# Optimization experiments

Hardware: AMD Instinct MI355X
Metric: run time of the kernel (lower is better)

The kernel has to match this reference:

```python
import jax, jax.numpy as jnp
import numpy as np

B, N, C, H, DFF = 4, 1024, 768, 12, 3072
D = C // H
EPS = 1e-5


def _layernorm(x, w, b, axes):
    mu = jnp.mean(x, axis=axes, keepdims=True)
    var = jnp.mean(jnp.square(x - mu), axis=axes, keepdims=True)
    return (x - mu) * jax.lax.rsqrt(var + EPS) * w + b


def setup_inputs() -> dict:
    key = jax.random.key(0)
    ks = jax.random.split(key, 8)
    s = lambda fan_in: 1.0 / np.sqrt(fan_in)
    return {
        'x': jax.random.normal(ks[0], (B, N, C), jnp.float32),
        'ln0_w': jnp.ones((C,), jnp.float32),
        'ln0_b': jnp.zeros((C,), jnp.float32),
        'qkv_w': jax.random.normal(ks[1], (3 * C, C), jnp.float32) * s(C),
        'qkv_b': jax.random.normal(ks[2], (3 * C,), jnp.float32) * 0.01,
        'proj_w': jax.random.normal(ks[3], (C, C), jnp.float32) * s(C),
        'proj_b': jax.random.normal(ks[4], (C,), jnp.float32) * 0.01,
        'attn_norm_w': jnp.ones((H, N, N), jnp.float32),
        'attn_norm_b': jnp.zeros((H, N, N), jnp.float32),
        'ln1_w': jnp.ones((C,), jnp.float32),
        'ln1_b': jnp.zeros((C,), jnp.float32),
        'fc1_w': jax.random.normal(ks[5], (DFF, C), jnp.float32) * s(C),
        'fc1_b': jax.random.normal(ks[6], (DFF,), jnp.float32) * 0.01,
        'fc2_w': jax.random.normal(ks[7], (C, DFF), jnp.float32) * s(DFF),
        'fc2_b': jnp.zeros((C,), jnp.float32),
    }


def reference(x, ln0_w, ln0_b, qkv_w, qkv_b, proj_w, proj_b,
              attn_norm_w, attn_norm_b, ln1_w, ln1_b,
              fc1_w, fc1_b, fc2_w, fc2_b):
    # pre-norm
    h = _layernorm(x, ln0_w, ln0_b, axes=-1)
    # qkv projection -> (3, B, H, N, D)
    qkv = (h @ qkv_w.T + qkv_b).reshape(B, N, 3, H, D).transpose(2, 0, 3, 1, 4)
    q, k, v = qkv[0], qkv[1], qkv[2]
    # grassmanian_point: project each head vector onto the unit sphere
    q = q / jnp.linalg.norm(q, axis=-1, keepdims=True)
    k = k / jnp.linalg.norm(k, axis=-1, keepdims=True)
    # sum_d (q_{id} k_{jd})^2  ==  (q^2) @ (k^2)^T   -- avoids (B,H,D,N,N) tensor
    attn = jnp.einsum('bhid,bhjd->bhij', jnp.square(q), jnp.square(k))
    # LayerNorm over (H, N, N) jointly per batch element
    attn = _layernorm(attn, attn_norm_w, attn_norm_b, axes=(1, 2, 3))
    out = jnp.einsum('bhij,bhjd->bhid', attn, v)
    out = out.transpose(0, 2, 1, 3).reshape(B, N, C)
    out = out @ proj_w.T + proj_b
    # residual + post-norm + FFN (dropout/drop_path are identity in eval)
    src = x + out
    src = _layernorm(src, ln1_w, ln1_b, axes=-1)
    ff = jax.nn.gelu(src @ fc1_w.T + fc1_b, approximate=False) @ fc2_w.T + fc2_b
    src = src + ff
    return src, attn
```

## Files before the change

kernel.cpp:

```cpp
#include <hip/hip_runtime.h>

typedef __bf16 bf16;
typedef __bf16 bf16x4 __attribute__((ext_vector_type(4)));
typedef __bf16 bf16x8 __attribute__((ext_vector_type(8)));
typedef float f32x4 __attribute__((ext_vector_type(4)));

#define DEVI __device__ __forceinline__

typedef const __attribute__((address_space(1))) void* gas1;
typedef __attribute__((address_space(3))) void* las3;

DEVI int xcd_chunk(int bid, int nwg)
{
  const int q = nwg >> 3, r = nwg & 7;
  const int xcd = bid & 7, rank = bid >> 3;
  return (xcd < r) ? xcd * (q + 1) + rank
                   : r * (q + 1) + (xcd - r) * q + rank;
}

DEVI void stage_tile(const bf16* g, int ld, char* lds, int bytes, int tid)
{
  const int wv = tid >> 6, lane = tid & 63;
  const char* gb = (const char*)g;
  const long rowb = (long)ld * 2;
  for (int off = wv * 1024; off < bytes; off += 4096) {
    const int o  = off + lane * 16;
    const int s  = o ^ (((o >> 7) & 7) << 4);
    const int r  = s >> 7;
    const int cb = s & 127;
    __builtin_amdgcn_global_load_lds((gas1)(gb + (long)r * rowb + cb),
                                     (las3)(lds + off), 16, 0, 0);
  }
}

template<int N> DEVI void waitvm()
{
  if constexpr (N == 8)      asm volatile("s_waitcnt vmcnt(8)" ::: "memory");
  else if constexpr (N == 6) asm volatile("s_waitcnt vmcnt(6)" ::: "memory");
  else if constexpr (N == 4) asm volatile("s_waitcnt vmcnt(4)" ::: "memory");
  else if constexpr (N == 2) asm volatile("s_waitcnt vmcnt(2)" ::: "memory");
  else                       asm volatile("s_waitcnt vmcnt(0)" ::: "memory");
}

DEVI void wave_lds_fence()
{
  asm volatile("s_waitcnt lgkmcnt(0)" ::: "memory");
  __builtin_amdgcn_sched_barrier(0);
}

struct EpiProj {
  const float* bias; const float* x; float* src;
  DEVI void operator()(int z, int row, int col, float v) const {
    const long i = (long)row * 768 + col;
    src[i] = v + bias[col] + x[i];
  }
};

struct EpiGelu {
  const float* bias; bf16* g;
  DEVI void operator()(int z, int row, int col, float v) const {
    const float t = v + bias[col];
    const float r = 0.5f * t * (1.0f + erff(t * 0.70710678118654752f));
    g[(long)row * 3072 + col] = (bf16)r;
  }
};

struct EpiOut {
  const float* bias; const float* lnf; float* outp;
  DEVI void operator()(int z, int row, int col, float v) const {
    const long i = (long)row * 768 + col;
    outp[i] = v + bias[col] + lnf[i];
  }
};

template<int BM, int BN, int WC, int FM, int FN, int WPE, class Epi>
__global__ __launch_bounds__(256, WPE) void gemm_k(
    const bf16* __restrict__ A, long abatch,
    const bf16* __restrict__ B, long bbatch,
    int lda, int ldb, int K, Epi epi)
{
  constexpr int BK = 64;
  constexpr int AB = BM * BK * 2, BB = BN * BK * 2;
  constexpr int BUFB = AB + BB;
  constexpr int LPS = BUFB / 4096;
  __shared__ char smem[2 * BUFB];

  const int tid = threadIdx.x, lane = tid & 63, wv = tid >> 6;
  const int wr = wv / WC, wc = wv % WC;
  const int NT = gridDim.x;
  const int nwg = NT * gridDim.y;
  const int wid = xcd_chunk(blockIdx.y * NT + blockIdx.x, nwg);
  const int mt = wid / NT, nt = wid % NT;
  const int z = blockIdx.z;
  const long abase = (long)z * abatch + (long)mt * BM * lda;
  const long bbase = (long)z * bbatch + (long)nt * BN * ldb;
  const int l15 = lane & 15;
  const int sw = (lane & 7) << 4;

  auto stage_all = [&](int buf, int kt) {
    char* base = smem + buf * BUFB;
    stage_tile(A + abase + kt, lda, base, AB, tid);
    stage_tile(B + bbase + kt, ldb, base + AB, BB, tid);
  };

  f32x4 acc[FM][FN];
#pragma unroll
  for (int m = 0; m < FM; ++m)
#pragma unroll
    for (int n = 0; n < FN; ++n) acc[m][n] = f32x4{0.f, 0.f, 0.f, 0.f};

  const int arow = wr * FM * 16, bcol = wc * FN * 16;
  const int T = K / BK;

  stage_all(0, 0);
  int cur = 0;
  for (int t = 0; t < T; ++t) {
    if (t + 1 < T) { stage_all(cur ^ 1, (t + 1) * BK); waitvm<LPS>(); }
    else           { waitvm<0>(); }
    __builtin_amdgcn_s_barrier();
    asm volatile("" ::: "memory");

    const char* As = smem + cur * BUFB;
    const char* Bs = As + AB;
#pragma unroll
    for (int ks = 0; ks < 2; ++ks) {
      const int ko = (ks * 64 + (lane >> 4) * 16) ^ sw;
      bf16x8 av[FM], bv[FN];
#pragma unroll
      for (int m = 0; m < FM; ++m)
        av[m] = *(const bf16x8*)(As + (arow + m * 16 + l15) * 128 + ko);
#pragma unroll
      for (int n = 0; n < FN; ++n)
        bv[n] = *(const bf16x8*)(Bs + (bcol + n * 16 + l15) * 128 + ko);
#pragma unroll
      for (int m = 0; m < FM; ++m)
#pragma unroll
        for (int n = 0; n < FN; ++n)
          acc[m][n] = __builtin_amdgcn_mfma_f32_16x16x32_bf16(av[m], bv[n], acc[m][n], 0, 0, 0);
    }
    asm volatile("s_waitcnt lgkmcnt(0)" ::: "memory");
    __builtin_amdgcn_s_barrier();
    asm volatile("" ::: "memory");
    cur ^= 1;
  }

#pragma unroll
  for (int m = 0; m < FM; ++m)
#pragma unroll
    for (int n = 0; n < FN; ++n)
#pragma unroll
      for (int r = 0; r < 4; ++r) {
        const int grow = mt * BM + arow + m * 16 + (lane >> 4) * 4 + r;
        const int gcol = nt * BN + bcol + n * 16 + l15;
        epi(z, grow, gcol, acc[m][n][r]);
      }
}

__global__ __launch_bounds__(256, 3) void gemm_qkv(
    const bf16* __restrict__ A, const bf16* __restrict__ B,
    const float* __restrict__ bias, bf16* __restrict__ q2h,
    bf16* __restrict__ k2h, bf16* __restrict__ vb)
{
  constexpr int BM = 128, BN = 64, BK = 64;
  constexpr int AB = BM * BK * 2, BB = BN * BK * 2;
  constexpr int BUFB = AB + BB;
  constexpr int LPS = BUFB / 4096;
  __shared__ char smem[2 * BUFB];
  __shared__ float rowsum[2][BM];

  const int tid = threadIdx.x, lane = tid & 63, wv = tid >> 6;
  const int wr = wv >> 1, wc = wv & 1;
  const int NT = 36;
  const int wid = xcd_chunk(blockIdx.y * NT + blockIdx.x, NT * 32);
  const int mt = wid / NT, nt = wid % NT;
  const int sec = nt / 12, h = nt - sec * 12;
  const long abase = (long)mt * BM * 768;
  const long bbase = (long)nt * BN * 768;
  const int l15 = lane & 15, lhi = lane >> 4;
  const int sw = (lane & 7) << 4;

  auto stage_all = [&](int buf, int kt) {
    char* base = smem + buf * BUFB;
    stage_tile(A + abase + kt, 768, base, AB, tid);
    stage_tile(B + bbase + kt, 768, base + AB, BB, tid);
  };

  f32x4 acc[4][2];
#pragma unroll
  for (int m = 0; m < 4; ++m)
#pragma unroll
    for (int n = 0; n < 2; ++n) acc[m][n] = f32x4{0.f, 0.f, 0.f, 0.f};

  const int arow = wr * 64, bcol = wc * 32;

  stage_all(0, 0);
  int cur = 0;
  for (int t = 0; t < 12; ++t) {
    if (t + 1 < 12) { stage_all(cur ^ 1, (t + 1) * BK); waitvm<LPS>(); }
    else            { waitvm<0>(); }
    __builtin_amdgcn_s_barrier();
    asm volatile("" ::: "memory");

    const char* As = smem + cur * BUFB;
    const char* Bs = As + AB;
#pragma unroll
    for (int ks = 0; ks < 2; ++ks) {
      const int ko = (ks * 64 + lhi * 16) ^ sw;
      bf16x8 av[4], bv[2];
#pragma unroll
      for (int m = 0; m < 4; ++m)
        av[m] = *(const bf16x8*)(As + (arow + m * 16 + l15) * 128 + ko);
#pragma unroll
      for (int n = 0; n < 2; ++n)
        bv[n] = *(const bf16x8*)(Bs + (bcol + n * 16 + l15) * 128 + ko);
#pragma unroll
      for (int m = 0; m < 4; ++m)
#pragma unroll
        for (int n = 0; n < 2; ++n)
          acc[m][n] = __builtin_amdgcn_mfma_f32_16x16x32_bf16(av[m], bv[n], acc[m][n], 0, 0, 0);
    }
    asm volatile("s_waitcnt lgkmcnt(0)" ::: "memory");
    __builtin_amdgcn_s_barrier();
    asm volatile("" ::: "memory");
    cur ^= 1;
  }

  float val[4][2][4];
#pragma unroll
  for (int m = 0; m < 4; ++m)
#pragma unroll
    for (int n = 0; n < 2; ++n)
#pragma unroll
      for (int r = 0; r < 4; ++r)
        val[m][n][r] = acc[m][n][r] + bias[nt * 64 + bcol + n * 16 + l15];

  if (sec < 2) {
#pragma unroll
    for (int m = 0; m < 4; ++m)
#pragma unroll
      for (int r = 0; r < 4; ++r) {
        float p = val[m][0][r] * val[m][0][r] + val[m][1][r] * val[m][1][r];
        p += __shfl_xor(p, 1);
        p += __shfl_xor(p, 2);
        p += __shfl_xor(p, 4);
        p += __shfl_xor(p, 8);
        if (l15 == 0) rowsum[wc][arow + m * 16 + lhi * 4 + r] = p;
      }
    __syncthreads();
    bf16* dst = (sec == 0) ? q2h : k2h;
#pragma unroll
    for (int m = 0; m < 4; ++m)
#pragma unroll
      for (int r = 0; r < 4; ++r) {
        const int row = arow + m * 16 + lhi * 4 + r;
        const float inv = 1.0f / (rowsum[0][row] + rowsum[1][row]);
        const int grow = mt * BM + row;
        const int b = grow >> 10, nn = grow & 1023;
        const long base = (((long)(b * 12 + h)) * 1024 + nn) * 64;
#pragma unroll
        for (int n = 0; n < 2; ++n) {
          const float v = val[m][n][r];
          dst[base + bcol + n * 16 + l15] = (bf16)(v * v * inv);
        }
      }
  } else {
#pragma unroll
    for (int m = 0; m < 4; ++m)
#pragma unroll
      for (int r = 0; r < 4; ++r) {
        const int grow = mt * BM + arow + m * 16 + lhi * 4 + r;
        const int b = grow >> 10, nn = grow & 1023;
        const long base = (((long)(b * 12 + h)) * 1024 + nn) * 64;
#pragma unroll
        for (int n = 0; n < 2; ++n)
          vb[base + bcol + n * 16 + l15] = (bf16)val[m][n][r];
      }
  }
}

__global__ __launch_bounds__(256, 3) void attn_fused(
    const bf16* __restrict__ q2h, const bf16* __restrict__ k2h,
    const bf16* __restrict__ vth, const float* __restrict__ stats,
    const float* __restrict__ wn, const float* __restrict__ bn,
    float* __restrict__ attn_out, bf16* __restrict__ oh)
{
  __shared__ char smem[49152];
  char* Qs  = smem;
  char* Ks0 = smem + 8192;
  char* Ks1 = smem + 16384;
  char* Vs0 = smem + 24576;
  char* Vs1 = smem + 32768;
  char* Pall = smem + 40960;

  const int tid = threadIdx.x, lane = tid & 63, wv = tid >> 6;
  const int wid = xcd_chunk(blockIdx.x, 768);
  const int b = wid & 3;
  const int mt = (wid >> 2) & 15;
  const int h = wid >> 6;
  const int zq = b * 12 + h;
  const float mu = stats[2 * b], rs = stats[2 * b + 1];
  const int l15 = lane & 15, lhi = lane >> 4;
  const int sw = (lane & 7) << 4;
  char* Ps = Pall + wv * 2048;

  const long zoff = (long)zq * 65536;
  stage_tile(q2h + zoff + (long)mt * 4096, 64, Qs, 8192, tid);
  stage_tile(k2h + zoff, 64, Ks0, 8192, tid);
  stage_tile(vth + zoff, 1024, Vs0, 8192, tid);
  __syncthreads();

  f32x4 oacc[4];
#pragma unroll
  for (int n = 0; n < 4; ++n) oacc[n] = f32x4{0.f, 0.f, 0.f, 0.f};

  for (int nt = 0; nt < 16; ++nt) {
    const int cur = nt & 1;
    char* Kc = cur ? Ks1 : Ks0;
    char* Vc = cur ? Vs1 : Vs0;
    char* Kn = cur ? Ks0 : Ks1;
    char* Vn = cur ? Vs0 : Vs1;

    if (nt + 1 < 16) {
      stage_tile(k2h + zoff + (long)(nt + 1) * 4096, 64, Kn, 8192, tid);
      stage_tile(vth + zoff + (nt + 1) * 64, 1024, Vn, 8192, tid);
    }
    f32x4 wreg[4], breg[4];
#pragma unroll
    for (int rr = 0; rr < 4; ++rr) {
      const long grow = (long)mt * 64 + wv * 16 + rr * 4 + lhi;
      const long gcol = (long)nt * 64 + l15 * 4;
      wreg[rr] = *(const f32x4*)&wn[((long)h * 1024 + grow) * 1024 + gcol];
      breg[rr] = *(const f32x4*)&bn[((long)h * 1024 + grow) * 1024 + gcol];
    }

    f32x4 acc[4];
#pragma unroll
    for (int n = 0; n < 4; ++n) acc[n] = f32x4{0.f, 0.f, 0.f, 0.f};
    __builtin_amdgcn_s_setprio(1);
#pragma unroll
    for (int ks = 0; ks < 2; ++ks) {
      const int ko = (ks * 64 + lhi * 16) ^ sw;
      const bf16x8 av = *(const bf16x8*)(Qs + (wv * 16 + l15) * 128 + ko);
#pragma unroll
      for (int n = 0; n < 4; ++n) {
        const bf16x8 bv = *(const bf16x8*)(Kc + (n * 16 + l15) * 128 + ko);
        acc[n] = __builtin_amdgcn_mfma_f32_16x16x32_bf16(av, bv, acc[n], 0, 0, 0);
      }
    }
    __builtin_amdgcn_s_setprio(0);
#pragma unroll
    for (int n = 0; n < 4; ++n)
#pragma unroll
      for (int r = 0; r < 4; ++r) {
        const int row = lhi * 4 + r;
        const int cb = (n * 32 + l15 * 2) ^ ((row & 7) << 4);
        *(bf16*)(Ps + row * 128 + cb) = (bf16)((acc[n][r] - mu) * rs);
      }
    wave_lds_fence();

#pragma unroll
    for (int rr = 0; rr < 4; ++rr) {
      const int row = rr * 4 + lhi;
      const int cb = (l15 * 8) ^ ((row & 7) << 4);
      const bf16x4 s4 = *(const bf16x4*)(Ps + row * 128 + cb);
      const long grow = (long)mt * 64 + wv * 16 + row;
      const long gcol = (long)nt * 64 + l15 * 4;
      f32x4 r4;
      bf16x4 h4;
#pragma unroll
      for (int e = 0; e < 4; ++e) {
        const float r = (float)s4[e] * wreg[rr][e] + breg[rr][e];
        r4[e] = r;
        h4[e] = (bf16)r;
      }
      *(f32x4*)&attn_out[((long)zq * 1024 + grow) * 1024 + gcol] = r4;
      *(bf16x4*)(Ps + row * 128 + cb) = h4;
    }
    wave_lds_fence();

    __builtin_amdgcn_s_setprio(1);
#pragma unroll
    for (int ks = 0; ks < 2; ++ks) {
      const int ko = (ks * 64 + lhi * 16) ^ sw;
      const bf16x8 av = *(const bf16x8*)(Ps + l15 * 128 + ko);
#pragma unroll
      for (int n = 0; n < 4; ++n) {
        const bf16x8 bv = *(const bf16x8*)(Vc + (n * 16 + l15) * 128 + ko);
        oacc[n] = __builtin_amdgcn_mfma_f32_16x16x32_bf16(av, bv, oacc[n], 0, 0, 0);
      }
    }
    __builtin_amdgcn_s_setprio(0);
    __syncthreads();
  }

#pragma unroll
  for (int n = 0; n < 4; ++n)
#pragma unroll
    for (int r = 0; r < 4; ++r) {
      const int row = mt * 64 + wv * 16 + lhi * 4 + r;
      const int col = n * 16 + l15;
      oh[((long)(b * 1024 + row)) * 768 + h * 64 + col] = (bf16)oacc[n][r];
    }
}

__global__ void cast_all(const float* __restrict__ qkvw, const float* __restrict__ projw,
                         const float* __restrict__ fc1w, const float* __restrict__ fc2w,
                         bf16* __restrict__ dq, bf16* __restrict__ dp,
                         bf16* __restrict__ d1, bf16* __restrict__ d2)
{
  const int i = blockIdx.x * 256 + threadIdx.x;
  const float* s; bf16* d; int off;
  if (i < 442368)       { s = qkvw; d = dq; off = i; }
  else if (i < 589824)  { s = projw; d = dp; off = i - 442368; }
  else if (i < 1179648) { s = fc1w; d = d1; off = i - 589824; }
  else                  { s = fc2w; d = d2; off = i - 1179648; }
  const f32x4 v = *(const f32x4*)&s[(long)off * 4];
  bf16x4 o;
#pragma unroll
  for (int j = 0; j < 4; ++j) o[j] = (bf16)v[j];
  *(bf16x4*)&d[(long)off * 4] = o;
}

__global__ __launch_bounds__(256) void ln_row(
    const float* __restrict__ in, const float* __restrict__ w,
    const float* __restrict__ b, bf16* __restrict__ outh,
    float* __restrict__ outf)
{
  __shared__ float red[256];
  const int row = blockIdx.x, tid = threadIdx.x;
  const float* p = in + (long)row * 768;
  const float v0 = p[tid], v1 = p[tid + 256], v2 = p[tid + 512];
  red[tid] = v0 + v1 + v2;
  __syncthreads();
  for (int st = 128; st > 0; st >>= 1) { if (tid < st) red[tid] += red[tid + st]; __syncthreads(); }
  const float mu = red[0] * (1.0f / 768.0f);
  __syncthreads();
  const float d0 = v0 - mu, d1 = v1 - mu, d2 = v2 - mu;
  red[tid] = d0 * d0 + d1 * d1 + d2 * d2;
  __syncthreads();
  for (int st = 128; st > 0; st >>= 1) { if (tid < st) red[tid] += red[tid + st]; __syncthreads(); }
  const float rs = rsqrtf(red[0] * (1.0f / 768.0f) + 1e-5f);
  const float dv[3] = {d0, d1, d2};
#pragma unroll
  for (int k = 0; k < 3; ++k) {
    const int c = tid + k * 256;
    const float h = dv[k] * rs * w[c] + b[c];
    outh[(long)row * 768 + c] = (bf16)h;
    if (outf) outf[(long)row * 768 + c] = h;
  }
}

__global__ __launch_bounds__(256) void transpose_v(
    const bf16* __restrict__ vb, bf16* __restrict__ vth)
{
  __shared__ float t[64][65];
  const int z = blockIdx.y, n0 = blockIdx.x * 64, tid = threadIdx.x;
  const bf16* srcp = vb + ((long)z * 1024 + n0) * 64;
  for (int e = tid * 8; e < 4096; e += 2048) {
    const bf16x8 v8 = *(const bf16x8*)&srcp[e];
    const int r = e >> 6, c = e & 63;
#pragma unroll
    for (int j = 0; j < 8; ++j) t[r][c + j] = (float)v8[j];
  }
  __syncthreads();
  for (int e = tid; e < 512; e += 256) {
    const int d = e >> 3, c0 = (e & 7) * 8;
    bf16x8 o;
#pragma unroll
    for (int j = 0; j < 8; ++j) o[j] = (bf16)t[c0 + j][d];
    *(bf16x8*)&vth[((long)z * 64 + d) * 1024 + n0 + c0] = o;
  }
}

__global__ __launch_bounds__(256) void stats_accum(
    const bf16* __restrict__ q2h, const bf16* __restrict__ k2h,
    float* __restrict__ Gq, float* __restrict__ Gk,
    float* __restrict__ Sq, float* __restrict__ Sk)
{
  __shared__ float rowbuf[8][128];
  const int tid = threadIdx.x;
  const int z = blockIdx.y;
  const long base = ((long)z * 1024 + (long)blockIdx.x * 128) * 64;
  const int tx = tid & 15, ty = tid >> 4;
  float gq[4][4] = {}, gk[4][4] = {};
  float sq = 0.f, sk = 0.f;
  for (int r0 = 0; r0 < 128; r0 += 8) {
    __syncthreads();
    {
      const int idx = tid * 4;
      const int rr = idx >> 7, cc = idx & 127;
      const long a = base + (long)(r0 + rr) * 64 + (cc & 63);
      const bf16x4 v4 = (cc < 64) ? *(const bf16x4*)&q2h[a]
                                  : *(const bf16x4*)&k2h[a];
#pragma unroll
      for (int j = 0; j < 4; ++j) rowbuf[rr][cc + j] = (float)v4[j];
    }
    __syncthreads();
#pragma unroll
    for (int r = 0; r < 8; ++r) {
      float qa[4], qe[4], ka[4], ke[4];
#pragma unroll
      for (int i = 0; i < 4; ++i) {
        qa[i] = rowbuf[r][ty * 4 + i]; qe[i] = rowbuf[r][tx * 4 + i];
        ka[i] = rowbuf[r][64 + ty * 4 + i]; ke[i] = rowbuf[r][64 + tx * 4 + i];
      }
#pragma unroll
      for (int i = 0; i < 4; ++i)
#pragma unroll
        for (int j = 0; j < 4; ++j) {
          gq[i][j] += qa[i] * qe[j];
          gk[i][j] += ka[i] * ke[j];
        }
    }
    if (tid < 128) {
      float s = 0.f;
#pragma unroll
      for (int r = 0; r < 8; ++r) s += rowbuf[r][tid];
      if (tid < 64) sq += s; else sk += s;
    }
  }
#pragma unroll
  for (int i = 0; i < 4; ++i)
#pragma unroll
    for (int j = 0; j < 4; ++j) {
      atomicAdd(&Gq[(long)z * 4096 + (ty * 4 + i) * 64 + tx * 4 + j], gq[i][j]);
      atomicAdd(&Gk[(long)z * 4096 + (ty * 4 + i) * 64 + tx * 4 + j], gk[i][j]);
    }
  if (tid < 64) atomicAdd(&Sq[z * 64 + tid], sq);
  else if (tid < 128) atomicAdd(&Sk[z * 64 + tid - 64], sk);
}

__global__ __launch_bounds__(256) void stats_final(
    const float* __restrict__ Gq, const float* __restrict__ Gk,
    const float* __restrict__ Sq, const float* __restrict__ Sk,
    float* __restrict__ stats)
{
  __shared__ double red[256];
  const int b = blockIdx.x, tid = threadIdx.x;
  double s2 = 0.0, s1 = 0.0;
  for (int h = 0; h < 12; ++h) {
    const float* gq = Gq + ((long)(b * 12 + h)) * 4096;
    const float* gk = Gk + ((long)(b * 12 + h)) * 4096;
    for (int i = tid; i < 4096; i += 256) s2 += (double)gq[i] * (double)gk[i];
    const float* sqp = Sq + (b * 12 + h) * 64;
    const float* skp = Sk + (b * 12 + h) * 64;
    for (int i = tid; i < 64; i += 256) s1 += (double)sqp[i] * (double)skp[i];
  }
  red[tid] = s2; __syncthreads();
  for (int st = 128; st > 0; st >>= 1) { if (tid < st) red[tid] += red[tid + st]; __syncthreads(); }
  const double S2 = red[0]; __syncthreads();
  red[tid] = s1; __syncthreads();
  for (int st = 128; st > 0; st >>= 1) { if (tid < st) red[tid] += red[tid + st]; __syncthreads(); }
  if (tid == 0) {
    const double S1 = red[0];
    const double cnt = 12.0 * 1024.0 * 1024.0;
    const double mean = S1 / cnt;
    const double var = S2 / cnt - mean * mean;
    stats[2 * b] = (float)mean;
    stats[2 * b + 1] = (float)(1.0 / sqrt(var + 1e-5));
  }
}

extern "C" void kernel_launch(void* const* d_in, const int* in_sizes, int n_in,
                              void* d_out, int out_size, void* d_ws, size_t ws_size,
                              hipStream_t stream)
{
  const float* x      = (const float*)d_in[0];
  const float* ln0_w  = (const float*)d_in[1];
  const float* ln0_b  = (const float*)d_in[2];
  const float* qkv_w  = (const float*)d_in[3];
  const float* qkv_b  = (const float*)d_in[4];
  const float* proj_w = (const float*)d_in[5];
  const float* proj_b = (const float*)d_in[6];
  const float* attn_w = (const float*)d_in[7];
  const float* attn_b = (const float*)d_in[8];
  const float* ln1_w  = (const float*)d_in[9];
  const float* ln1_b  = (const float*)d_in[10];
  const float* fc1_w  = (const float*)d_in[11];
  const float* fc1_b  = (const float*)d_in[12];
  const float* fc2_w  = (const float*)d_in[13];
  const float* fc2_b  = (const float*)d_in[14];

  float* out_src  = (float*)d_out;
  float* out_attn = out_src + 4L * 1024 * 768;

  char* p = (char*)d_ws;
  auto take = [&](long bytes) -> char* {
    char* r = p;
    p += (bytes + 255) & ~255L;
    return r;
  };
  bf16* qkvw_h = (bf16*)take(3538944);
  bf16* projw_h = (bf16*)take(1179648);
  bf16* fc1w_h = (bf16*)take(4718592);
  bf16* fc2w_h = (bf16*)take(4718592);
  char* regB = take(12582912);
  bf16* hh = (bf16*)regB;
  float* src = (float*)regB;
  char* regC = take(37748736);
  bf16* gact = (bf16*)regC;
  float* ln1f = (float*)(regC + 25165824);
  bf16* q2h = (bf16*)take(6291456);
  bf16* k2h = (bf16*)take(6291456);
  bf16* vb  = (bf16*)take(6291456);
  bf16* vth = (bf16*)take(6291456);
  bf16* oh  = (bf16*)take(6291456);
  bf16* h1v = (bf16*)take(6291456);
  float* Gq = (float*)take(786432);
  float* Gk = (float*)take(786432);
  float* Sq = (float*)take(12288);
  float* Sk = (float*)take(12288);
  float* stats = (float*)take(256);

  const dim3 blk(256);

  (void)hipMemsetAsync((void*)Gq, 0, 786432 * 2 + 12288 * 2 + 256, stream);

  cast_all<<<dim3(1769472 / 256), blk, 0, stream>>>(
      qkv_w, proj_w, fc1_w, fc2_w, qkvw_h, projw_h, fc1w_h, fc2w_h);

  ln_row<<<dim3(4096), blk, 0, stream>>>(x, ln0_w, ln0_b, hh, nullptr);

  gemm_qkv<<<dim3(36, 32), blk, 0, stream>>>(
      hh, qkvw_h, qkv_b, q2h, k2h, vb);

  transpose_v<<<dim3(16, 48), blk, 0, stream>>>(vb, vth);
  stats_accum<<<dim3(8, 48), blk, 0, stream>>>(q2h, k2h, Gq, Gk, Sq, Sk);
  stats_final<<<dim3(4), blk, 0, stream>>>(Gq, Gk, Sq, Sk, stats);

  attn_fused<<<dim3(768), blk, 0, stream>>>(
      q2h, k2h, vth, stats, attn_w, attn_b, out_attn, oh);

  gemm_k<128, 64, 2, 4, 2, 3, EpiProj><<<dim3(12, 32, 1), blk, 0, stream>>>(
      oh, 0, projw_h, 0, 768, 768, 768, EpiProj{proj_b, x, src});

  ln_row<<<dim3(4096), blk, 0, stream>>>(src, ln1_w, ln1_b, h1v, ln1f);

  gemm_k<128, 64, 2, 4, 2, 3, EpiGelu><<<dim3(48, 32, 1), blk, 0, stream>>>(
      h1v, 0, fc1w_h, 0, 768, 768, 768, EpiGelu{fc1_b, gact});

  gemm_k<128, 64, 2, 4, 2, 3, EpiOut><<<dim3(12, 32, 1), blk, 0, stream>>>(
      gact, 0, fc2w_h, 0, 3072, 3072, 3072, EpiOut{fc2_b, ln1f, out_src});
}
```

Measured before the change: 380.3 us.

## Prefetch attn-norm weights one tile ahead and fuse affine into MFMA layout

The attention-LayerNorm weight and bias are now loaded in the MFMA accumulator layout, one key tile ahead, into registers. The affine transform and the fp32 attn output store then happen directly from accumulators. This removes an LDS round-trip and a wave fence, and hides global load latency behind the QK MFMAs. In exchange it uses scalar, non-vectorized global loads and stores with 64-byte row segments, and adds 64 extra live registers.

New measurement: 386.9 us. About the same (+1.7%).

```diff
diff --git a/kernel.cpp b/kernel.cpp
--- a/kernel.cpp
+++ b/kernel.cpp
@@ -303,10 +303,27 @@
   const int sw = (lane & 7) << 4;
   char* Ps = Pall + wv * 2048;
 
+  const long wb_row0 = (long)mt * 64 + wv * 16 + lhi * 4;
+
   const long zoff = (long)zq * 65536;
   stage_tile(q2h + zoff + (long)mt * 4096, 64, Qs, 8192, tid);
   stage_tile(k2h + zoff, 64, Ks0, 8192, tid);
   stage_tile(vth + zoff, 1024, Vs0, 8192, tid);
+
+  auto load_wb = [&](int nt, float (*wreg)[4], float (*breg)[4]) {
+#pragma unroll
+    for (int n = 0; n < 4; ++n)
+#pragma unroll
+      for (int r = 0; r < 4; ++r) {
+        const long idx = ((long)h * 1024 + wb_row0 + r) * 1024
+                       + nt * 64 + n * 16 + l15;
+        wreg[n][r] = wn[idx];
+        breg[n][r] = bn[idx];
+      }
+  };
+
+  float wcur[4][4], bcur[4][4];
+  load_wb(0, wcur, bcur);
   __syncthreads();
 
   f32x4 oacc[4];
@@ -320,17 +337,11 @@
     char* Kn = cur ? Ks0 : Ks1;
     char* Vn = cur ? Vs0 : Vs1;
 
+    float wnx[4][4], bnx[4][4];
     if (nt + 1 < 16) {
       stage_tile(k2h + zoff + (long)(nt + 1) * 4096, 64, Kn, 8192, tid);
       stage_tile(vth + zoff + (nt + 1) * 64, 1024, Vn, 8192, tid);
-    }
-    f32x4 wreg[4], breg[4];
-#pragma unroll
-    for (int rr = 0; rr < 4; ++rr) {
-      const long grow = (long)mt * 64 + wv * 16 + rr * 4 + lhi;
-      const long gcol = (long)nt * 64 + l15 * 4;
-      wreg[rr] = *(const f32x4*)&wn[((long)h * 1024 + grow) * 1024 + gcol];
-      breg[rr] = *(const f32x4*)&bn[((long)h * 1024 + grow) * 1024 + gcol];
+      load_wb(nt + 1, wnx, bnx);
     }
 
     f32x4 acc[4];
@@ -348,34 +359,18 @@
       }
     }
     __builtin_amdgcn_s_setprio(0);
+
 #pragma unroll
     for (int n = 0; n < 4; ++n)
 #pragma unroll
       for (int r = 0; r < 4; ++r) {
+        const float rv = (acc[n][r] - mu) * rs * wcur[n][r] + bcur[n][r];
+        const long arow = (long)zq * 1024 + wb_row0 + r;
+        attn_out[arow * 1024 + nt * 64 + n * 16 + l15] = rv;
         const int row = lhi * 4 + r;
         const int cb = (n * 32 + l15 * 2) ^ ((row & 7) << 4);
-        *(bf16*)(Ps + row * 128 + cb) = (bf16)((acc[n][r] - mu) * rs);
-      }
-    wave_lds_fence();
-
-#pragma unroll
-    for (int rr = 0; rr < 4; ++rr) {
-      const int row = rr * 4 + lhi;
-      const int cb = (l15 * 8) ^ ((row & 7) << 4);
-      const bf16x4 s4 = *(const bf16x4*)(Ps + row * 128 + cb);
-      const long grow = (long)mt * 64 + wv * 16 + row;
-      const long gcol = (long)nt * 64 + l15 * 4;
-      f32x4 r4;
-      bf16x4 h4;
-#pragma unroll
-      for (int e = 0; e < 4; ++e) {
-        const float r = (float)s4[e] * wreg[rr][e] + breg[rr][e];
-        r4[e] = r;
-        h4[e] = (bf16)r;
-      }
-      *(f32x4*)&attn_out[((long)zq * 1024 + grow) * 1024 + gcol] = r4;
-      *(bf16x4*)(Ps + row * 128 + cb) = h4;
-    }
+        *(bf16*)(Ps + row * 128 + cb) = (bf16)rv;
+      }
     wave_lds_fence();
 
     __builtin_amdgcn_s_setprio(1);
@@ -391,6 +386,16 @@
     }
     __builtin_amdgcn_s_setprio(0);
     __syncthreads();
+
+    if (nt + 1 < 16) {
+#pragma unroll
+      for (int n = 0; n < 4; ++n)
+#pragma unroll
+        for (int r = 0; r < 4; ++r) {
+          wcur[n][r] = wnx[n][r];
+          bcur[n][r] = bnx[n][r];
+        }
+    }
   }
 
 #pragma unroll
```

## Fuse V transpose into QKV GEMM epilogue and prefetch attn-norm weights

Applied to the files above, without the earlier changes.

The QKV GEMM epilogue for the V section now transposes its tile through LDS and writes V directly in the (d, n) layout. This removes the separate transpose_v kernel and the intermediate vb buffer round-trip. In attn_fused, the attention-LayerNorm weight and bias for the next tile are loaded one iteration ahead. The end-of-iteration __syncthreads is replaced with a partial vmcnt wait plus barrier so those loads can stay in flight. This costs extra registers and relies on the waitvm count matching the load ordering.

New measurement: 364.9 us. 1.04x faster.

```diff
diff --git a/kernel.cpp b/kernel.cpp
--- a/kernel.cpp
+++ b/kernel.cpp
@@ -159,7 +159,7 @@
 __global__ __launch_bounds__(256, 3) void gemm_qkv(
     const bf16* __restrict__ A, const bf16* __restrict__ B,
     const float* __restrict__ bias, bf16* __restrict__ q2h,
-    bf16* __restrict__ k2h, bf16* __restrict__ vb)
+    bf16* __restrict__ k2h, bf16* __restrict__ vth)
 {
   constexpr int BM = 128, BN = 64, BK = 64;
   constexpr int AB = BM * BK * 2, BB = BN * BK * 2;
@@ -264,17 +264,27 @@
         }
       }
   } else {
+    bf16* T = (bf16*)smem;
 #pragma unroll
     for (int m = 0; m < 4; ++m)
 #pragma unroll
-      for (int r = 0; r < 4; ++r) {
-        const int grow = mt * BM + arow + m * 16 + lhi * 4 + r;
-        const int b = grow >> 10, nn = grow & 1023;
-        const long base = (((long)(b * 12 + h)) * 1024 + nn) * 64;
-#pragma unroll
-        for (int n = 0; n < 2; ++n)
-          vb[base + bcol + n * 16 + l15] = (bf16)val[m][n][r];
-      }
+      for (int n = 0; n < 2; ++n)
+#pragma unroll
+        for (int r = 0; r < 4; ++r) {
+          const int row = arow + m * 16 + lhi * 4 + r;
+          const int col = bcol + n * 16 + l15;
+          T[col * 144 + row] = (bf16)val[m][n][r];
+        }
+    __syncthreads();
+    const int bq = mt >> 3, nn0 = (mt & 7) * 128;
+    const long basez = ((long)(bq * 12 + h) * 64) * 1024;
+#pragma unroll
+    for (int it = 0; it < 4; ++it) {
+      const int flat = it * 2048 + tid * 8;
+      const int d = flat >> 7, c = flat & 127;
+      const bf16x8 o = *(const bf16x8*)&T[d * 144 + c];
+      *(bf16x8*)&vth[basez + (long)d * 1024 + nn0 + c] = o;
+    }
   }
 }
 
@@ -304,6 +314,19 @@
   char* Ps = Pall + wv * 2048;
 
   const long zoff = (long)zq * 65536;
+
+  auto load_wb = [&](int nt, f32x4* wreg, f32x4* breg) {
+#pragma unroll
+    for (int rr = 0; rr < 4; ++rr) {
+      const long grow = (long)mt * 64 + wv * 16 + rr * 4 + lhi;
+      const long gcol = (long)nt * 64 + l15 * 4;
+      wreg[rr] = *(const f32x4*)&wn[((long)h * 1024 + grow) * 1024 + gcol];
+      breg[rr] = *(const f32x4*)&bn[((long)h * 1024 + grow) * 1024 + gcol];
+    }
+  };
+
+  f32x4 wcur[4], bcur[4];
+  load_wb(0, wcur, bcur);
   stage_tile(q2h + zoff + (long)mt * 4096, 64, Qs, 8192, tid);
   stage_tile(k2h + zoff, 64, Ks0, 8192, tid);
   stage_tile(vth + zoff, 1024, Vs0, 8192, tid);
@@ -320,17 +343,11 @@
     char* Kn = cur ? Ks0 : Ks1;
     char* Vn = cur ? Vs0 : Vs1;
 
+    f32x4 wnx[4], bnx[4];
     if (nt + 1 < 16) {
+      load_wb(nt + 1, wnx, bnx);
       stage_tile(k2h + zoff + (long)(nt + 1) * 4096, 64, Kn, 8192, tid);
       stage_tile(vth + zoff + (nt + 1) * 64, 1024, Vn, 8192, tid);
-    }
-    f32x4 wreg[4], breg[4];
-#pragma unroll
-    for (int rr = 0; rr < 4; ++rr) {
-      const long grow = (long)mt * 64 + wv * 16 + rr * 4 + lhi;
-      const long gcol = (long)nt * 64 + l15 * 4;
-      wreg[rr] = *(const f32x4*)&wn[((long)h * 1024 + grow) * 1024 + gcol];
-      breg[rr] = *(const f32x4*)&bn[((long)h * 1024 + grow) * 1024 + gcol];
     }
 
     f32x4 acc[4];
@@ -369,7 +386,7 @@
       bf16x4 h4;
 #pragma unroll
       for (int e = 0; e < 4; ++e) {
-        const float r = (float)s4[e] * wreg[rr][e] + breg[rr][e];
+        const float r = (float)s4[e] * wcur[rr][e] + bcur[rr][e];
         r4[e] = r;
         h4[e] = (bf16)r;
       }
@@ -390,7 +407,14 @@
       }
     }
     __builtin_amdgcn_s_setprio(0);
-    __syncthreads();
+    waitvm<4>();
+    __builtin_amdgcn_s_barrier();
+    asm volatile("" ::: "memory");
+
+    if (nt + 1 < 16) {
+#pragma unroll
+      for (int rr = 0; rr < 4; ++rr) { wcur[rr] = wnx[rr]; bcur[rr] = bnx[rr]; }
+    }
   }
 
 #pragma unroll
@@ -447,28 +471,6 @@
     const float h = dv[k] * rs * w[c] + b[c];
     outh[(long)row * 768 + c] = (bf16)h;
     if (outf) outf[(long)row * 768 + c] = h;
-  }
-}
-
-__global__ __launch_bounds__(256) void transpose_v(
-    const bf16* __restrict__ vb, bf16* __restrict__ vth)
-{
-  __shared__ float t[64][65];
-  const int z = blockIdx.y, n0 = blockIdx.x * 64, tid = threadIdx.x;
-  const bf16* srcp = vb + ((long)z * 1024 + n0) * 64;
-  for (int e = tid * 8; e < 4096; e += 2048) {
-    const bf16x8 v8 = *(const bf16x8*)&srcp[e];
-    const int r = e >> 6, c = e & 63;
-#pragma unroll
-    for (int j = 0; j < 8; ++j) t[r][c + j] = (float)v8[j];
-  }
-  __syncthreads();
-  for (int e = tid; e < 512; e += 256) {
-    const int d = e >> 3, c0 = (e & 7) * 8;
-    bf16x8 o;
-#pragma unroll
-    for (int j = 0; j < 8; ++j) o[j] = (bf16)t[c0 + j][d];
-    *(bf16x8*)&vth[((long)z * 64 + d) * 1024 + n0 + c0] = o;
   }
 }
 
@@ -602,7 +604,6 @@
   float* ln1f = (float*)(regC + 25165824);
   bf16* q2h = (bf16*)take(6291456);
   bf16* k2h = (bf16*)take(6291456);
-  bf16* vb  = (bf16*)take(6291456);
   bf16* vth = (bf16*)take(6291456);
   bf16* oh  = (bf16*)take(6291456);
   bf16* h1v = (bf16*)take(6291456);
@@ -622,9 +623,8 @@
   ln_row<<<dim3(4096), blk, 0, stream>>>(x, ln0_w, ln0_b, hh, nullptr);
 
   gemm_qkv<<<dim3(36, 32), blk, 0, stream>>>(
-      hh, qkvw_h, qkv_b, q2h, k2h, vb);
-
-  transpose_v<<<dim3(16, 48), blk, 0, stream>>>(vb, vth);
+      hh, qkvw_h, qkv_b, q2h, k2h, vth);
+
   stats_accum<<<dim3(8, 48), blk, 0, stream>>>(q2h, k2h, Gq, Gk, Sq, Sk);
   stats_final<<<dim3(4), blk, 0, stream>>>(Gq, Gk, Sq, Sk, stats);
 
```
